# Kernel optimization log

Hardware: AMD Instinct MI355X
Metric: run time of the kernel (lower is better)

Reference implementation:

```python
import jax, jax.numpy as jnp
import numpy as np

K = 4096   # infeatures
N = 11008  # outfeatures
T = 8192   # tokens (batch*seq)
GROUP = 32
E8M0_BIAS = 127
E2M1_VALS = jnp.array([0.0, 0.5, 1.0, 1.5, 2.0, 3.0, 4.0, 6.0], dtype=jnp.float32)


def setup_inputs() -> dict:
    key = jax.random.key(0)
    k1, k2, k3, k4 = jax.random.split(key, 4)
    x = jax.random.normal(k1, (T, K), dtype=jnp.float32)
    # packed fp4: 8 nibbles per int32 along the in-feature axis -> [K//8, N]
    weight_packed = jax.random.randint(k2, (K // 8, N), 0, 2147483647, dtype=jnp.int32)
    # e8m0 exponents near the bias so 2^(e-127) stays well-conditioned in fp32
    weight_scale_e8m0 = 112 + jax.random.randint(k3, (K // GROUP, N), 0, 30, dtype=jnp.int32)
    bias = jax.random.normal(k4, (N,), dtype=jnp.float32)
    return {"x": x, "weight_packed": weight_packed,
            "weight_scale_e8m0": weight_scale_e8m0, "bias": bias}


def dequantize_weight(weight_packed, weight_scale_e8m0):
    # unpack 8 fp4 nibbles per int32: nibble j -> in-feature row r*8 + j
    shifts = (jnp.arange(8, dtype=jnp.int32) * 4)[None, :, None]       # [1,8,1]
    nib = (weight_packed[:, None, :] >> shifts) & 0xF                   # [K//8,8,N]
    mag = E2M1_VALS[nib & 0x7]                                           # e2m1 magnitude
    sign = jnp.where((nib >> 3) & 1 == 1, -1.0, 1.0).astype(jnp.float32)
    w = (mag * sign).reshape(K, N)
    # per-group e8m0 scale: 2^(e - 127), groups of 32 along in-features
    scale = jnp.exp2((weight_scale_e8m0 - E8M0_BIAS).astype(jnp.float32))  # [K//32,N]
    w = (w.reshape(K // GROUP, GROUP, N) * scale[:, None, :]).reshape(K, N)
    return w


def reference(x, weight_packed, weight_scale_e8m0, bias):
    w = dequantize_weight(weight_packed, weight_scale_e8m0)  # [K, N]
    return x @ w + bias                                       # [T, N]
```

## Files before the change

kernel.cpp:

```cpp
#include <hip/hip_runtime.h>


#define TDIM 8192
#define KDIM 4096
#define NDIM 11008

typedef __attribute__((ext_vector_type(8))) short short8;
typedef __attribute__((ext_vector_type(8))) unsigned short ushort8;
typedef __attribute__((ext_vector_type(4))) float f32x4;

__device__ __forceinline__ unsigned short f2bf(float f) {
    unsigned int u = __float_as_uint(f);
    u += 0x7FFFu + ((u >> 16) & 1u);
    return (unsigned short)(u >> 16);
}

__device__ __forceinline__ unsigned short nib2bf(unsigned int v, int e) {
    unsigned int m3 = v & 7u;
    if (m3 == 0u) return 0;
    unsigned int s = (v & 8u) << 12;
    unsigned int E = (unsigned int)e + (m3 >> 1) - 1u;
    unsigned int man = (m3 >= 2u) ? ((m3 & 1u) << 6) : 0u;
    return (unsigned short)(s | (E << 7) | man);
}

__device__ __forceinline__ void gload_lds16(const void* g, void* l) {
    __builtin_amdgcn_global_load_lds(
        (const __attribute__((address_space(1))) void*)g,
        (__attribute__((address_space(3))) void*)l, 16, 0, 0);
}

__global__ __launch_bounds__(256) void prepass(const float* __restrict__ x,
                                               unsigned short* __restrict__ xbf,
                                               const int* __restrict__ wp,
                                               const int* __restrict__ wse,
                                               unsigned short* __restrict__ wt) {
    __shared__ int sT[64][65];
    const int tid = threadIdx.x;
    if (blockIdx.x < 16384) {
        size_t i = ((size_t)blockIdx.x * 256 + tid) * 8;
        float4 v0 = *(const float4*)(x + i);
        float4 v1 = *(const float4*)(x + i + 4);
        ushort8 r;
        r[0] = f2bf(v0.x); r[1] = f2bf(v0.y); r[2] = f2bf(v0.z); r[3] = f2bf(v0.w);
        r[4] = f2bf(v1.x); r[5] = f2bf(v1.y); r[6] = f2bf(v1.z); r[7] = f2bf(v1.w);
        *(ushort8*)(xbf + i) = r;
        return;
    }
    const int bb = blockIdx.x - 16384;
    const int n0 = (bb % 172) * 64;
    const int r0 = (bb / 172) * 64;

    #pragma unroll
    for (int i = 0; i < 16; ++i) {
        int idx = i * 256 + tid;
        int r = idx >> 6, n = idx & 63;
        sT[r][n] = wp[(size_t)(r0 + r) * NDIM + n0 + n];
    }
    __syncthreads();
    #pragma unroll
    for (int i = 0; i < 16; ++i) {
        int idx = i * 256 + tid;
        int n = idx >> 6, r = idx & 63;
        unsigned int p = (unsigned int)sT[r][n];
        int e = wse[(size_t)((r0 + r) >> 2) * NDIM + n0 + n];
        ushort8 o;
        #pragma unroll
        for (int j = 0; j < 8; ++j) o[j] = nib2bf((p >> (4 * j)) & 0xFu, e);
        *(ushort8*)(wt + (size_t)(n0 + n) * KDIM + (size_t)(r0 + r) * 8) = o;
    }
}

#define STG_A(GOFF, C, HK)                                                                  \
    do {                                                                                    \
        gload_lds16(pA0 + (GOFF), ldsW + (C)*32768 + (HK)*8192);                            \
        gload_lds16(pA1 + (GOFF), ldsW + (C)*32768 + (HK)*8192 + 4096);                     \
    } while (0)

#define STG_B(GOFF, C, HK)                                                                  \
    do {                                                                                    \
        gload_lds16(pB0 + (GOFF), ldsW + (C)*32768 + 16384 + (HK)*8192);                    \
        if constexpr (NF == 4)                                                              \
            gload_lds16(pB1 + (GOFF), ldsW + (C)*32768 + 16384 + (HK)*8192 + 4096);         \
    } while (0)

#define RD_A(CB, KS, MH, DST)                                                                      \
    DST[0] = *(const short8*)(ldsC + (CB)*65536 + (KS)*16384 + ((MH)*4 + 0)*1024 + aoff);          \
    DST[1] = *(const short8*)(ldsC + (CB)*65536 + (KS)*16384 + ((MH)*4 + 1)*1024 + aoff);          \
    DST[2] = *(const short8*)(ldsC + (CB)*65536 + (KS)*16384 + ((MH)*4 + 2)*1024 + aoff);          \
    DST[3] = *(const short8*)(ldsC + (CB)*65536 + (KS)*16384 + ((MH)*4 + 3)*1024 + aoff);

#define RD_B(CB, KS, DST)                                                                          \
    DST[0] = *(const short8*)(ldsC + (CB)*65536 + 32768 + (KS)*16384 + 0*1024 + boff);             \
    DST[1] = *(const short8*)(ldsC + (CB)*65536 + 32768 + (KS)*16384 + 1*1024 + boff);             \
    if constexpr (NF == 4) {                                                                       \
        DST[2] = *(const short8*)(ldsC + (CB)*65536 + 32768 + (KS)*16384 + 2*1024 + boff);         \
        DST[3] = *(const short8*)(ldsC + (CB)*65536 + 32768 + (KS)*16384 + 3*1024 + boff);         \
    }

#define CLUSTER(A, B, MH)                                                      \
    __builtin_amdgcn_s_setprio(1);                                             \
    _Pragma("unroll")                                                          \
    for (int i_ = 0; i_ < 4; ++i_) {                                           \
        _Pragma("unroll")                                                      \
        for (int n_ = 0; n_ < NF; ++n_)                                        \
            acc[(MH)*4 + i_][n_] = __builtin_amdgcn_mfma_f32_16x16x32_bf16(    \
                A[i_], B[n_], acc[(MH)*4 + i_][n_], 0, 0, 0);                  \
    }                                                                          \
    __builtin_amdgcn_s_setprio(0);

#define VWAIT_STEADY()                                                         \
    do { if constexpr (NF == 4) asm volatile("s_waitcnt vmcnt(4)" ::: "memory"); \
         else                   asm volatile("s_waitcnt vmcnt(3)" ::: "memory"); } while (0)

#define BODY(T, C)                                                             \
    do {                                                                       \
                       \
        if ((T) < 63) STG_A(96, (C)^1, 1);                                     \
        RD_A((C), 0, 1, aY)                                                    \
        CLUSTER(aX, bX, 0)                                                     \
                \
        if ((T) < 63) STG_B(96, (C)^1, 1);                                     \
        RD_B((C), 1, bY)                                                       \
        RD_A((C), 1, 0, aX)                                                    \
        CLUSTER(aY, bX, 1)                                                     \
             \
        if ((T) < 63) VWAIT_STEADY();                                          \
        __builtin_amdgcn_s_barrier();                                          \
              \
        if ((T) < 62) STG_A(128, (C), 0);                                      \
        RD_A((C), 1, 1, aY)                                                    \
        CLUSTER(aX, bY, 0)                                                     \
                       \
        if ((T) < 62) STG_B(128, (C), 0);                                      \
        if ((T) < 63) { RD_B((C)^1, 0, bX) RD_A((C)^1, 0, 0, aX) }             \
        CLUSTER(aY, bY, 1)                                                     \
        if ((T) < 62)       VWAIT_STEADY();                                    \
        else if ((T) == 62) asm volatile("s_waitcnt vmcnt(0)" ::: "memory");   \
        __builtin_amdgcn_s_barrier();                                          \
        pA0 += 64; pA1 += 64; pB0 += 64; pB1 += 64;                            \
    } while (0)

template<int NF>
__global__ __launch_bounds__(512, 1) void gemm256(const unsigned short* __restrict__ xbf,
                                                  const unsigned short* __restrict__ wt,
                                                  const float* __restrict__ bias,
                                                  float* __restrict__ out) {
    __shared__ __attribute__((aligned(16))) unsigned short lds[2][2][16384];
    const int tid = threadIdx.x;
    const int l = tid & 63, wid = tid >> 6;
    const int wm = wid >> 2, wn = wid & 3;

    int b = blockIdx.x;
    int swz, half = 0;
    if constexpr (NF == 4) {
        swz = (b & 7) * 160 + (b >> 3);
    } else {
        int js = (b & 7) * 24 + (b >> 3);
        swz = 1280 + (js >> 1);
        half = js & 1;
    }
    int band = swz / 344;
    int r = swz % 344;
    int st = r >> 5; if (st > 10) st = 10;
    int ii = r - (st << 5);
    int w = (st < 10) ? 4 : 3;
    const int bm0 = (band * 8 + ii / w) * 256;
    const int bn0 = (st * 4 + ii % w) * 256 + half * 128;

    int rs0, ks0, rs1, ks1;
    {
        int chunk = wid * 64 + l;
        int cin = chunk & 63;
        cin ^= ((cin >> 5) & 1) << 1;
        rs0 = (chunk >> 6) * 16 + (cin >> 2);
        ks0 = (cin & 3) * 8;
        chunk = 512 + wid * 64 + l;
        cin = chunk & 63;
        cin ^= ((cin >> 5) & 1) << 1;
        rs1 = (chunk >> 6) * 16 + (cin >> 2);
        ks1 = (cin & 3) * 8;
    }

    const unsigned short* pA0 = xbf + (size_t)(bm0 + rs0) * KDIM + ks0;
    const unsigned short* pA1 = xbf + (size_t)(bm0 + rs1) * KDIM + ks1;
    const unsigned short* pB0 = wt + (size_t)(bn0 + rs0) * KDIM + ks0;
    const unsigned short* pB1 = wt + (size_t)(bn0 + rs1) * KDIM + ks1;

    unsigned short* ldsW = &lds[0][0][0] + wid * 512;
    const char* ldsC = (const char*)&lds[0][0][0];

    const int lbyte = (((l & 15) * 64 + ((l >> 4) << 4))) ^ ((l & 8) << 2);
    const int aoff = wm * 8192 + lbyte;
    const int boff = wn * (NF * 1024) + lbyte;

    f32x4 acc[8][4] = {};
    short8 aX[4], aY[4], bX[4], bY[4];

    STG_A(0, 0, 0);   STG_B(0, 0, 0);
    STG_A(32, 0, 1);  STG_B(32, 0, 1);
    STG_A(64, 1, 0);  STG_B(64, 1, 0);
    if constexpr (NF == 4) asm volatile("s_waitcnt vmcnt(4)" ::: "memory");
    else                   asm volatile("s_waitcnt vmcnt(3)" ::: "memory");
    __builtin_amdgcn_s_barrier();
    RD_B(0, 0, bX)
    RD_A(0, 0, 0, aX)

    for (int tt = 0; tt < 32; ++tt) {
        BODY(2 * tt, 0);
        BODY(2 * tt + 1, 1);
    }

    const int crow = (l >> 4) * 4, ccol = l & 15;
    #pragma unroll
    for (int nf = 0; nf < NF; ++nf) {
        int col = bn0 + wn * (NF * 16) + nf * 16 + ccol;
        float bv = bias[col];
        #pragma unroll
        for (int m = 0; m < 8; ++m) {
            int row0 = bm0 + wm * 128 + m * 16 + crow;
            #pragma unroll
            for (int j2 = 0; j2 < 4; ++j2)
                __builtin_nontemporal_store(acc[m][nf][j2] + bv,
                                            &out[(size_t)(row0 + j2) * NDIM + col]);
        }
    }
}

__global__ __launch_bounds__(256, 2) void gemm_fused(const float* __restrict__ x,
                                                     const int* __restrict__ wp,
                                                     const int* __restrict__ wse,
                                                     const float* __restrict__ bias,
                                                     float* __restrict__ out) {
    __shared__ __attribute__((aligned(16))) unsigned short lA[128 * 64];
    __shared__ __attribute__((aligned(16))) unsigned short lB[128 * 64];
    const int tid = threadIdx.x;
    const int l = tid & 63, wid = tid >> 6;
    const int bn0 = blockIdx.x * 128, bm0 = blockIdx.y * 128;
    const int wm = wid >> 1, wn = wid & 1;

    f32x4 acc[4][4] = {};

    for (int k0 = 0; k0 < KDIM; k0 += 64) {
        float4 av0[4], av1[4];
        unsigned int bp[4];
        int be[4];
        #pragma unroll
        for (int i = 0; i < 4; ++i) {
            int seg = i * 256 + tid;
            int row = seg >> 3, kseg = seg & 7;
            const float4* p = (const float4*)(x + (size_t)(bm0 + row) * KDIM + k0 + kseg * 8);
            av0[i] = p[0]; av1[i] = p[1];
        }
        #pragma unroll
        for (int i = 0; i < 4; ++i) {
            int idx = i * 256 + tid;
            int ln = idx & 127, lr = idx >> 7;
            bp[i] = ((const unsigned int*)wp)[(size_t)(k0 / 8 + lr) * NDIM + bn0 + ln];
            be[i] = wse[(size_t)((k0 + lr * 8) >> 5) * NDIM + bn0 + ln];
        }
        #pragma unroll
        for (int i = 0; i < 4; ++i) {
            int seg = i * 256 + tid;
            int row = seg >> 3, kseg = seg & 7;
            ushort8 r;
            r[0] = f2bf(av0[i].x); r[1] = f2bf(av0[i].y); r[2] = f2bf(av0[i].z); r[3] = f2bf(av0[i].w);
            r[4] = f2bf(av1[i].x); r[5] = f2bf(av1[i].y); r[6] = f2bf(av1[i].z); r[7] = f2bf(av1[i].w);
            *(ushort8*)&lA[row * 64 + kseg * 8] = r;
        }
        #pragma unroll
        for (int i = 0; i < 4; ++i) {
            int idx = i * 256 + tid;
            int ln = idx & 127, lr = idx >> 7;
            unsigned int p = bp[i];
            int e = be[i];
            ushort8 r;
            #pragma unroll
            for (int j = 0; j < 8; ++j) r[j] = nib2bf((p >> (4 * j)) & 0xFu, e);
            *(ushort8*)&lB[ln * 64 + lr * 8] = r;
        }
        __syncthreads();
        #pragma unroll
        for (int kc = 0; kc < 2; ++kc) {
            short8 a[4], bb[4];
            #pragma unroll
            for (int f = 0; f < 4; ++f) {
                a[f] = *(const short8*)&lA[(wm * 64 + f * 16 + (l & 15)) * 64 + kc * 32 + (l >> 4) * 8];
                bb[f] = *(const short8*)&lB[(wn * 64 + f * 16 + (l & 15)) * 64 + kc * 32 + (l >> 4) * 8];
            }
            #pragma unroll
            for (int fm = 0; fm < 4; ++fm)
                #pragma unroll
                for (int fn = 0; fn < 4; ++fn)
                    acc[fm][fn] = __builtin_amdgcn_mfma_f32_16x16x32_bf16(a[fm], bb[fn], acc[fm][fn], 0, 0, 0);
        }
        __syncthreads();
    }

    const int crow = (l >> 4) * 4, ccol = l & 15;
    #pragma unroll
    for (int fn = 0; fn < 4; ++fn) {
        int col = bn0 + wn * 64 + fn * 16 + ccol;
        float bv = bias[col];
        #pragma unroll
        for (int fm = 0; fm < 4; ++fm) {
            int row0 = bm0 + wm * 64 + fm * 16 + crow;
            #pragma unroll
            for (int j = 0; j < 4; ++j)
                out[(size_t)(row0 + j) * NDIM + col] = acc[fm][fn][j] + bv;
        }
    }
}

extern "C" void kernel_launch(void* const* d_in, const int* in_sizes, int n_in,
                              void* d_out, int out_size, void* d_ws, size_t ws_size,
                              hipStream_t stream) {
    (void)in_sizes; (void)n_in; (void)out_size;
    const float* x = (const float*)d_in[0];
    const int* wp = (const int*)d_in[1];
    const int* wse = (const int*)d_in[2];
    const float* bias = (const float*)d_in[3];
    float* out = (float*)d_out;

    const size_t xbf_bytes = (size_t)TDIM * KDIM * 2;
    const size_t wt_bytes = (size_t)NDIM * KDIM * 2;

    if (ws_size >= xbf_bytes + wt_bytes) {
        unsigned short* xbf = (unsigned short*)d_ws;
        unsigned short* wt = (unsigned short*)((char*)d_ws + xbf_bytes);
        prepass<<<dim3(16384 + 1376), dim3(256), 0, stream>>>(x, xbf, wp, wse, wt);
        gemm256<4><<<dim3(1280), dim3(512), 0, stream>>>(xbf, wt, bias, out);
        gemm256<2><<<dim3(192), dim3(512), 0, stream>>>(xbf, wt, bias, out);
    } else {
        hipLaunchKernelGGL(gemm_fused, dim3(NDIM / 128, TDIM / 128), dim3(256), 0, stream, x, wp, wse, bias, out);
    }
}
```

Measured before the change: 673.9 us.

## Switch main GEMM to 32x32x16 MFMA with re-laid-out LDS tiles

Replaces the 16x16x32 bf16 MFMA inner product with the 32x32x16 variant. The global-to-LDS staging layout, the LDS read addressing, the k-substep schedule (four substeps per stage instead of two halves) and the epilogue mapping all change to match. The aim is fewer MFMA issues and fewer LDS fragment reads per unit of work, because the larger tile gives more reuse per operand load. The risks are LDS bank conflicts under the new layout, index bugs in the new mapping, and a strided epilogue store pattern.

```diff
diff --git a/kernel.cpp b/kernel.cpp
--- a/kernel.cpp
+++ b/kernel.cpp
@@ -8,6 +8,7 @@
 typedef __attribute__((ext_vector_type(8))) short short8;
 typedef __attribute__((ext_vector_type(8))) unsigned short ushort8;
 typedef __attribute__((ext_vector_type(4))) float f32x4;
+typedef __attribute__((ext_vector_type(16))) float f32x16;
 
 __device__ __forceinline__ unsigned short f2bf(float f) {
     unsigned int u = __float_as_uint(f);
@@ -71,41 +72,43 @@
     }
 }
 
-#define STG_A(GOFF, C, HK)                                                                  \
-    do {                                                                                    \
-        gload_lds16(pA0 + (GOFF), ldsW + (C)*32768 + (HK)*8192);                            \
-        gload_lds16(pA1 + (GOFF), ldsW + (C)*32768 + (HK)*8192 + 4096);                     \
+#define STG_A(GOFF, C, HK)                                                                   \
+    do {                                                                                     \
+        gload_lds16(pA0 + (GOFF), ldsL + (C)*32768 + (HK)*8192 + (wid*2 + 0)*512);           \
+        gload_lds16(pA1 + (GOFF), ldsL + (C)*32768 + (HK)*8192 + (wid*2 + 1)*512);           \
     } while (0)
 
-#define STG_B(GOFF, C, HK)                                                                  \
-    do {                                                                                    \
-        gload_lds16(pB0 + (GOFF), ldsW + (C)*32768 + 16384 + (HK)*8192);                    \
-        if constexpr (NF == 4)                                                              \
-            gload_lds16(pB1 + (GOFF), ldsW + (C)*32768 + 16384 + (HK)*8192 + 4096);         \
+#define STG_B(GOFF, C, HK)                                                                   \
+    do {                                                                                     \
+        if constexpr (NF == 4) {                                                             \
+            gload_lds16(pB0 + (GOFF), ldsL + (C)*32768 + 16384 + (HK)*8192 + (wid*2 + 0)*512); \
+            gload_lds16(pB1 + (GOFF), ldsL + (C)*32768 + 16384 + (HK)*8192 + (wid*2 + 1)*512); \
+        } else {                                                                             \
+            gload_lds16(pB0 + (GOFF), ldsL + (C)*32768 + 16384 + (HK)*4096 + wid*512);       \
+        }                                                                                    \
     } while (0)
 
-#define RD_A(CB, KS, MH, DST)                                                                      \
-    DST[0] = *(const short8*)(ldsC + (CB)*65536 + (KS)*16384 + ((MH)*4 + 0)*1024 + aoff);          \
-    DST[1] = *(const short8*)(ldsC + (CB)*65536 + (KS)*16384 + ((MH)*4 + 1)*1024 + aoff);          \
-    DST[2] = *(const short8*)(ldsC + (CB)*65536 + (KS)*16384 + ((MH)*4 + 2)*1024 + aoff);          \
-    DST[3] = *(const short8*)(ldsC + (CB)*65536 + (KS)*16384 + ((MH)*4 + 3)*1024 + aoff);
-
-#define RD_B(CB, KS, DST)                                                                          \
-    DST[0] = *(const short8*)(ldsC + (CB)*65536 + 32768 + (KS)*16384 + 0*1024 + boff);             \
-    DST[1] = *(const short8*)(ldsC + (CB)*65536 + 32768 + (KS)*16384 + 1*1024 + boff);             \
-    if constexpr (NF == 4) {                                                                       \
-        DST[2] = *(const short8*)(ldsC + (CB)*65536 + 32768 + (KS)*16384 + 2*1024 + boff);         \
-        DST[3] = *(const short8*)(ldsC + (CB)*65536 + 32768 + (KS)*16384 + 3*1024 + boff);         \
-    }
-
-#define CLUSTER(A, B, MH)                                                      \
+#define RD_A(CB, S, DST)                                                                             \
+    DST[0] = *(const short8*)(ldsC + (CB)*65536 + ((S)>>1)*16384 + ((S)&1)*8192 + (wm*4 + 0)*1024 + lbyte); \
+    DST[1] = *(const short8*)(ldsC + (CB)*65536 + ((S)>>1)*16384 + ((S)&1)*8192 + (wm*4 + 1)*1024 + lbyte); \
+    DST[2] = *(const short8*)(ldsC + (CB)*65536 + ((S)>>1)*16384 + ((S)&1)*8192 + (wm*4 + 2)*1024 + lbyte); \
+    DST[3] = *(const short8*)(ldsC + (CB)*65536 + ((S)>>1)*16384 + ((S)&1)*8192 + (wm*4 + 3)*1024 + lbyte);
+
+#define RD_B(CB, S, DST)                                                                             \
+    DST[0] = *(const short8*)(ldsC + (CB)*65536 + 32768 + ((S)>>1)*(NF*4096) + ((S)&1)*(NF*2048)     \
+                              + (wn*(NF/2) + 0)*1024 + lbyte);                                       \
+    if constexpr (NF == 4)                                                                           \
+        DST[1] = *(const short8*)(ldsC + (CB)*65536 + 32768 + ((S)>>1)*(NF*4096) + ((S)&1)*(NF*2048) \
+                                  + (wn*2 + 1)*1024 + lbyte);
+
+#define CLUSTER(A, B)                                                          \
     __builtin_amdgcn_s_setprio(1);                                             \
     _Pragma("unroll")                                                          \
-    for (int i_ = 0; i_ < 4; ++i_) {                                           \
+    for (int m_ = 0; m_ < 4; ++m_) {                                           \
         _Pragma("unroll")                                                      \
-        for (int n_ = 0; n_ < NF; ++n_)                                        \
-            acc[(MH)*4 + i_][n_] = __builtin_amdgcn_mfma_f32_16x16x32_bf16(    \
-                A[i_], B[n_], acc[(MH)*4 + i_][n_], 0, 0, 0);                  \
+        for (int n_ = 0; n_ < NF/2; ++n_)                                      \
+            acc[m_][n_] = __builtin_amdgcn_mfma_f32_32x32x16_bf16(             \
+                A[m_], B[n_], acc[m_][n_], 0, 0, 0);                           \
     }                                                                          \
     __builtin_amdgcn_s_setprio(0);
 
@@ -115,26 +118,28 @@
 
 #define BODY(T, C)                                                             \
     do {                                                                       \
-                       \
+                          \
         if ((T) < 63) STG_A(96, (C)^1, 1);                                     \
-        RD_A((C), 0, 1, aY)                                                    \
-        CLUSTER(aX, bX, 0)                                                     \
-                \
+        RD_A((C), 1, aY)                                                       \
+        RD_B((C), 1, bY)                                                       \
+        CLUSTER(aX, bX)                                                        \
+                          \
         if ((T) < 63) STG_B(96, (C)^1, 1);                                     \
-        RD_B((C), 1, bY)                                                       \
-        RD_A((C), 1, 0, aX)                                                    \
-        CLUSTER(aY, bX, 1)                                                     \
-             \
+        RD_A((C), 2, aX)                                                       \
+        RD_B((C), 2, bX)                                                       \
+        CLUSTER(aY, bY)                                                        \
+                  \
         if ((T) < 63) VWAIT_STEADY();                                          \
         __builtin_amdgcn_s_barrier();                                          \
+         \
+        if ((T) < 62) STG_A(128, (C), 0);                                      \
+        RD_A((C), 3, aY)                                                       \
+        RD_B((C), 3, bY)                                                       \
+        CLUSTER(aX, bX)                                                        \
               \
-        if ((T) < 62) STG_A(128, (C), 0);                                      \
-        RD_A((C), 1, 1, aY)                                                    \
-        CLUSTER(aX, bY, 0)                                                     \
-                       \
         if ((T) < 62) STG_B(128, (C), 0);                                      \
-        if ((T) < 63) { RD_B((C)^1, 0, bX) RD_A((C)^1, 0, 0, aX) }             \
-        CLUSTER(aY, bY, 1)                                                     \
+        if ((T) < 63) { RD_A((C)^1, 0, aX) RD_B((C)^1, 0, bX) }                \
+        CLUSTER(aY, bY)                                                        \
         if ((T) < 62)       VWAIT_STEADY();                                    \
         else if ((T) == 62) asm volatile("s_waitcnt vmcnt(0)" ::: "memory");   \
         __builtin_amdgcn_s_barrier();                                          \
@@ -168,61 +173,54 @@
     const int bm0 = (band * 8 + ii / w) * 256;
     const int bn0 = (st * 4 + ii % w) * 256 + half * 128;
 
-    int rs0, ks0, rs1, ks1;
-    {
-        int chunk = wid * 64 + l;
-        int cin = chunk & 63;
-        cin ^= ((cin >> 5) & 1) << 1;
-        rs0 = (chunk >> 6) * 16 + (cin >> 2);
-        ks0 = (cin & 3) * 8;
-        chunk = 512 + wid * 64 + l;
-        cin = chunk & 63;
-        cin ^= ((cin >> 5) & 1) << 1;
-        rs1 = (chunk >> 6) * 16 + (cin >> 2);
-        ks1 = (cin & 3) * 8;
-    }
-
-    const unsigned short* pA0 = xbf + (size_t)(bm0 + rs0) * KDIM + ks0;
-    const unsigned short* pA1 = xbf + (size_t)(bm0 + rs1) * KDIM + ks1;
-    const unsigned short* pB0 = wt + (size_t)(bn0 + rs0) * KDIM + ks0;
-    const unsigned short* pB1 = wt + (size_t)(bn0 + rs1) * KDIM + ks1;
-
-    unsigned short* ldsW = &lds[0][0][0] + wid * 512;
+    const int lo = l >> 2;
+    const int hi = (l & 3) ^ (((l >> 5) & 1) << 1);
+    const int row_l = (hi & 1) * 16 + lo;
+    const int k8o = (hi >> 1) * 8;
+
+    const unsigned short* pA0 = xbf + (size_t)(bm0 + ((wid*2+0) & 7)*32 + row_l) * KDIM + ((wid*2+0) >> 3)*16 + k8o;
+    const unsigned short* pA1 = xbf + (size_t)(bm0 + ((wid*2+1) & 7)*32 + row_l) * KDIM + ((wid*2+1) >> 3)*16 + k8o;
+    int cb0, sh0;
+    if constexpr (NF == 4) { cb0 = (wid*2) & 7; sh0 = (wid*2) >> 3; }
+    else                   { cb0 = wid & 3;     sh0 = wid >> 2; }
+    const unsigned short* pB0 = wt + (size_t)(bn0 + cb0*32 + row_l) * KDIM + sh0*16 + k8o;
+    const unsigned short* pB1 = wt + (size_t)(bn0 + ((wid*2+1) & 7)*32 + row_l) * KDIM + ((wid*2+1) >> 3)*16 + k8o;
+
+    unsigned short* ldsL = &lds[0][0][0];
     const char* ldsC = (const char*)&lds[0][0][0];
 
-    const int lbyte = (((l & 15) * 64 + ((l >> 4) << 4))) ^ ((l & 8) << 2);
-    const int aoff = wm * 8192 + lbyte;
-    const int boff = wn * (NF * 1024) + lbyte;
-
-    f32x4 acc[8][4] = {};
-    short8 aX[4], aY[4], bX[4], bY[4];
+    const int lbyte = ((l & 15) * 64 + ((l >> 4) << 4)) ^ ((l & 8) << 2);
+
+    f32x16 acc[4][NF/2] = {};
+    short8 aX[4], aY[4], bX[2], bY[2];
 
     STG_A(0, 0, 0);   STG_B(0, 0, 0);
     STG_A(32, 0, 1);  STG_B(32, 0, 1);
     STG_A(64, 1, 0);  STG_B(64, 1, 0);
-    if constexpr (NF == 4) asm volatile("s_waitcnt vmcnt(4)" ::: "memory");
-    else                   asm volatile("s_waitcnt vmcnt(3)" ::: "memory");
+    VWAIT_STEADY();
     __builtin_amdgcn_s_barrier();
+    RD_A(0, 0, aX)
     RD_B(0, 0, bX)
-    RD_A(0, 0, 0, aX)
 
     for (int tt = 0; tt < 32; ++tt) {
         BODY(2 * tt, 0);
         BODY(2 * tt + 1, 1);
     }
 
-    const int crow = (l >> 4) * 4, ccol = l & 15;
+    const int ecol = l & 31, erow = (l >> 5) * 4;
     #pragma unroll
-    for (int nf = 0; nf < NF; ++nf) {
-        int col = bn0 + wn * (NF * 16) + nf * 16 + ccol;
+    for (int nb = 0; nb < NF/2; ++nb) {
+        int col = bn0 + wn * (NF * 16) + nb * 32 + ecol;
         float bv = bias[col];
         #pragma unroll
-        for (int m = 0; m < 8; ++m) {
-            int row0 = bm0 + wm * 128 + m * 16 + crow;
-            #pragma unroll
-            for (int j2 = 0; j2 < 4; ++j2)
-                __builtin_nontemporal_store(acc[m][nf][j2] + bv,
-                                            &out[(size_t)(row0 + j2) * NDIM + col]);
+        for (int mb = 0; mb < 4; ++mb) {
+            int rowbase = bm0 + wm * 128 + mb * 32 + erow;
+            #pragma unroll
+            for (int reg = 0; reg < 16; ++reg) {
+                int row = rowbase + (reg & 3) + 8 * (reg >> 2);
+                __builtin_nontemporal_store(acc[mb][nb][reg] + bv,
+                                            &out[(size_t)row * NDIM + col]);
+            }
         }
     }
 }
```

Result: slower. 874.8 us (+29.8%).

## Replace 256x256 two-kernel GEMM with single 128x128 tile GEMM at two blocks per CU

Applied to the files above, without the earlier changes.

Swaps the 512-thread 256x256 tile GEMM, which needed a second launch for the 128-wide N remainder, for one 256-thread 128x128 tile kernel that covers all of N in a single launch with two blocks per CU. The per-iteration schedule is simplified so each half-step issues A and B staging together, reads one A and B fragment set, and runs one 4x4 MFMA cluster. The goal is to drop the extra launch and tail handling and to let two resident blocks hide latency. In exchange, arithmetic intensity per tile is halved, so global and LDS traffic per FLOP roughly doubles and the kernel may become more bandwidth-bound.

```diff
diff --git a/kernel.cpp b/kernel.cpp
--- a/kernel.cpp
+++ b/kernel.cpp
@@ -73,109 +73,87 @@
 
 #define STG_A(GOFF, C, HK)                                                                  \
     do {                                                                                    \
-        gload_lds16(pA0 + (GOFF), ldsW + (C)*32768 + (HK)*8192);                            \
-        gload_lds16(pA1 + (GOFF), ldsW + (C)*32768 + (HK)*8192 + 4096);                     \
+        gload_lds16(pA0 + (GOFF), ldsW + (C)*16384 + (HK)*4096);                            \
+        gload_lds16(pA1 + (GOFF), ldsW + (C)*16384 + (HK)*4096 + 2048);                     \
     } while (0)
 
 #define STG_B(GOFF, C, HK)                                                                  \
     do {                                                                                    \
-        gload_lds16(pB0 + (GOFF), ldsW + (C)*32768 + 16384 + (HK)*8192);                    \
-        if constexpr (NF == 4)                                                              \
-            gload_lds16(pB1 + (GOFF), ldsW + (C)*32768 + 16384 + (HK)*8192 + 4096);         \
+        gload_lds16(pB0 + (GOFF), ldsW + (C)*16384 + 8192 + (HK)*4096);                     \
+        gload_lds16(pB1 + (GOFF), ldsW + (C)*16384 + 8192 + (HK)*4096 + 2048);              \
     } while (0)
 
-#define RD_A(CB, KS, MH, DST)                                                                      \
-    DST[0] = *(const short8*)(ldsC + (CB)*65536 + (KS)*16384 + ((MH)*4 + 0)*1024 + aoff);          \
-    DST[1] = *(const short8*)(ldsC + (CB)*65536 + (KS)*16384 + ((MH)*4 + 1)*1024 + aoff);          \
-    DST[2] = *(const short8*)(ldsC + (CB)*65536 + (KS)*16384 + ((MH)*4 + 2)*1024 + aoff);          \
-    DST[3] = *(const short8*)(ldsC + (CB)*65536 + (KS)*16384 + ((MH)*4 + 3)*1024 + aoff);
+#define RD_A(CB, KS, DST)                                                                          \
+    DST[0] = *(const short8*)(ldsC + (CB)*32768 + (KS)*8192 + (wm*4 + 0)*1024 + lbyte);            \
+    DST[1] = *(const short8*)(ldsC + (CB)*32768 + (KS)*8192 + (wm*4 + 1)*1024 + lbyte);            \
+    DST[2] = *(const short8*)(ldsC + (CB)*32768 + (KS)*8192 + (wm*4 + 2)*1024 + lbyte);            \
+    DST[3] = *(const short8*)(ldsC + (CB)*32768 + (KS)*8192 + (wm*4 + 3)*1024 + lbyte);
 
 #define RD_B(CB, KS, DST)                                                                          \
-    DST[0] = *(const short8*)(ldsC + (CB)*65536 + 32768 + (KS)*16384 + 0*1024 + boff);             \
-    DST[1] = *(const short8*)(ldsC + (CB)*65536 + 32768 + (KS)*16384 + 1*1024 + boff);             \
-    if constexpr (NF == 4) {                                                                       \
-        DST[2] = *(const short8*)(ldsC + (CB)*65536 + 32768 + (KS)*16384 + 2*1024 + boff);         \
-        DST[3] = *(const short8*)(ldsC + (CB)*65536 + 32768 + (KS)*16384 + 3*1024 + boff);         \
-    }
-
-#define CLUSTER(A, B, MH)                                                      \
+    DST[0] = *(const short8*)(ldsC + (CB)*32768 + 16384 + (KS)*8192 + (wn*4 + 0)*1024 + lbyte);    \
+    DST[1] = *(const short8*)(ldsC + (CB)*32768 + 16384 + (KS)*8192 + (wn*4 + 1)*1024 + lbyte);    \
+    DST[2] = *(const short8*)(ldsC + (CB)*32768 + 16384 + (KS)*8192 + (wn*4 + 2)*1024 + lbyte);    \
+    DST[3] = *(const short8*)(ldsC + (CB)*32768 + 16384 + (KS)*8192 + (wn*4 + 3)*1024 + lbyte);
+
+#define CLUSTER(A, B)                                                          \
     __builtin_amdgcn_s_setprio(1);                                             \
     _Pragma("unroll")                                                          \
     for (int i_ = 0; i_ < 4; ++i_) {                                           \
         _Pragma("unroll")                                                      \
-        for (int n_ = 0; n_ < NF; ++n_)                                        \
-            acc[(MH)*4 + i_][n_] = __builtin_amdgcn_mfma_f32_16x16x32_bf16(    \
-                A[i_], B[n_], acc[(MH)*4 + i_][n_], 0, 0, 0);                  \
+        for (int n_ = 0; n_ < 4; ++n_)                                         \
+            acc[i_][n_] = __builtin_amdgcn_mfma_f32_16x16x32_bf16(             \
+                A[i_], B[n_], acc[i_][n_], 0, 0, 0);                           \
     }                                                                          \
     __builtin_amdgcn_s_setprio(0);
 
-#define VWAIT_STEADY()                                                         \
-    do { if constexpr (NF == 4) asm volatile("s_waitcnt vmcnt(4)" ::: "memory"); \
-         else                   asm volatile("s_waitcnt vmcnt(3)" ::: "memory"); } while (0)
-
 #define BODY(T, C)                                                             \
     do {                                                                       \
-                       \
-        if ((T) < 63) STG_A(96, (C)^1, 1);                                     \
-        RD_A((C), 0, 1, aY)                                                    \
-        CLUSTER(aX, bX, 0)                                                     \
-                \
-        if ((T) < 63) STG_B(96, (C)^1, 1);                                     \
+                        \
+        if ((T) < 63) { STG_A(96, (C)^1, 1); STG_B(96, (C)^1, 1); }            \
+        RD_A((C), 1, aY)                                                       \
         RD_B((C), 1, bY)                                                       \
-        RD_A((C), 1, 0, aX)                                                    \
-        CLUSTER(aY, bX, 1)                                                     \
-             \
-        if ((T) < 63) VWAIT_STEADY();                                          \
+        CLUSTER(aX, bX)                                                        \
+                 \
+        if ((T) < 63) asm volatile("s_waitcnt vmcnt(4)" ::: "memory");         \
         __builtin_amdgcn_s_barrier();                                          \
-              \
-        if ((T) < 62) STG_A(128, (C), 0);                                      \
-        RD_A((C), 1, 1, aY)                                                    \
-        CLUSTER(aX, bY, 0)                                                     \
-                       \
-        if ((T) < 62) STG_B(128, (C), 0);                                      \
-        if ((T) < 63) { RD_B((C)^1, 0, bX) RD_A((C)^1, 0, 0, aX) }             \
-        CLUSTER(aY, bY, 1)                                                     \
-        if ((T) < 62)       VWAIT_STEADY();                                    \
+          \
+        if ((T) < 62) { STG_A(128, (C), 0); STG_B(128, (C), 0); }              \
+        if ((T) < 63) { RD_A((C)^1, 0, aX) RD_B((C)^1, 0, bX) }                \
+        CLUSTER(aY, bY)                                                        \
+                 \
+        if ((T) < 62)       asm volatile("s_waitcnt vmcnt(4)" ::: "memory");   \
         else if ((T) == 62) asm volatile("s_waitcnt vmcnt(0)" ::: "memory");   \
         __builtin_amdgcn_s_barrier();                                          \
         pA0 += 64; pA1 += 64; pB0 += 64; pB1 += 64;                            \
     } while (0)
 
-template<int NF>
-__global__ __launch_bounds__(512, 1) void gemm256(const unsigned short* __restrict__ xbf,
+__global__ __launch_bounds__(256, 2) void gemm128(const unsigned short* __restrict__ xbf,
                                                   const unsigned short* __restrict__ wt,
                                                   const float* __restrict__ bias,
                                                   float* __restrict__ out) {
-    __shared__ __attribute__((aligned(16))) unsigned short lds[2][2][16384];
+    __shared__ __attribute__((aligned(16))) unsigned short lds[2][16384];
     const int tid = threadIdx.x;
     const int l = tid & 63, wid = tid >> 6;
-    const int wm = wid >> 2, wn = wid & 3;
+    const int wm = wid >> 1, wn = wid & 1;
 
     int b = blockIdx.x;
-    int swz, half = 0;
-    if constexpr (NF == 4) {
-        swz = (b & 7) * 160 + (b >> 3);
-    } else {
-        int js = (b & 7) * 24 + (b >> 3);
-        swz = 1280 + (js >> 1);
-        half = js & 1;
-    }
-    int band = swz / 344;
-    int r = swz % 344;
-    int st = r >> 5; if (st > 10) st = 10;
-    int ii = r - (st << 5);
-    int w = (st < 10) ? 4 : 3;
-    const int bm0 = (band * 8 + ii / w) * 256;
-    const int bn0 = (st * 4 + ii % w) * 256 + half * 128;
+    int swz = (b & 7) * 688 + (b >> 3);
+    int band = swz / 688;
+    int r = swz % 688;
+    int st = r >> 6; if (st > 10) st = 10;
+    int ii = r - (st << 6);
+    int w = (st < 10) ? 8 : 6;
+    const int bm0 = (band * 8 + ii / w) * 128;
+    const int bn0 = (st * 8 + ii % w) * 128;
 
     int rs0, ks0, rs1, ks1;
     {
-        int chunk = wid * 64 + l;
+        int chunk = tid;
         int cin = chunk & 63;
         cin ^= ((cin >> 5) & 1) << 1;
         rs0 = (chunk >> 6) * 16 + (cin >> 2);
         ks0 = (cin & 3) * 8;
-        chunk = 512 + wid * 64 + l;
+        chunk = 256 + tid;
         cin = chunk & 63;
         cin ^= ((cin >> 5) & 1) << 1;
         rs1 = (chunk >> 6) * 16 + (cin >> 2);
@@ -187,24 +165,21 @@
     const unsigned short* pB0 = wt + (size_t)(bn0 + rs0) * KDIM + ks0;
     const unsigned short* pB1 = wt + (size_t)(bn0 + rs1) * KDIM + ks1;
 
-    unsigned short* ldsW = &lds[0][0][0] + wid * 512;
-    const char* ldsC = (const char*)&lds[0][0][0];
+    unsigned short* ldsW = &lds[0][0] + wid * 512;
+    const char* ldsC = (const char*)&lds[0][0];
 
     const int lbyte = (((l & 15) * 64 + ((l >> 4) << 4))) ^ ((l & 8) << 2);
-    const int aoff = wm * 8192 + lbyte;
-    const int boff = wn * (NF * 1024) + lbyte;
-
-    f32x4 acc[8][4] = {};
+
+    f32x4 acc[4][4] = {};
     short8 aX[4], aY[4], bX[4], bY[4];
 
     STG_A(0, 0, 0);   STG_B(0, 0, 0);
     STG_A(32, 0, 1);  STG_B(32, 0, 1);
     STG_A(64, 1, 0);  STG_B(64, 1, 0);
-    if constexpr (NF == 4) asm volatile("s_waitcnt vmcnt(4)" ::: "memory");
-    else                   asm volatile("s_waitcnt vmcnt(3)" ::: "memory");
+    asm volatile("s_waitcnt vmcnt(4)" ::: "memory");
     __builtin_amdgcn_s_barrier();
+    RD_A(0, 0, aX)
     RD_B(0, 0, bX)
-    RD_A(0, 0, 0, aX)
 
     for (int tt = 0; tt < 32; ++tt) {
         BODY(2 * tt, 0);
@@ -213,12 +188,12 @@
 
     const int crow = (l >> 4) * 4, ccol = l & 15;
     #pragma unroll
-    for (int nf = 0; nf < NF; ++nf) {
-        int col = bn0 + wn * (NF * 16) + nf * 16 + ccol;
+    for (int nf = 0; nf < 4; ++nf) {
+        int col = bn0 + wn * 64 + nf * 16 + ccol;
         float bv = bias[col];
         #pragma unroll
-        for (int m = 0; m < 8; ++m) {
-            int row0 = bm0 + wm * 128 + m * 16 + crow;
+        for (int m = 0; m < 4; ++m) {
+            int row0 = bm0 + wm * 64 + m * 16 + crow;
             #pragma unroll
             for (int j2 = 0; j2 < 4; ++j2)
                 __builtin_nontemporal_store(acc[m][nf][j2] + bv,
@@ -329,8 +304,7 @@
         unsigned short* xbf = (unsigned short*)d_ws;
         unsigned short* wt = (unsigned short*)((char*)d_ws + xbf_bytes);
         prepass<<<dim3(16384 + 1376), dim3(256), 0, stream>>>(x, xbf, wp, wse, wt);
-        gemm256<4><<<dim3(1280), dim3(512), 0, stream>>>(xbf, wt, bias, out);
-        gemm256<2><<<dim3(192), dim3(512), 0, stream>>>(xbf, wt, bias, out);
+        gemm128<<<dim3((TDIM / 128) * (NDIM / 128)), dim3(256), 0, stream>>>(xbf, wt, bias, out);
     } else {
         hipLaunchKernelGGL(gemm_fused, dim3(NDIM / 128, TDIM / 128), dim3(256), 0, stream, x, wp, wse, bias, out);
     }
```

New measurement: 883.4 us. 31.1% more time.
